# Kernel optimization log

Measured on AMD Instinct MI355X. Metric: run time of the kernel, lower is better.

## Reference

```python
import jax, jax.numpy as jnp
import numpy as np

S, N, F, H, O = 64, 4096, 32, 64, 2  # seq_len, n_nodes, nfeat, nhid, nout


def setup_inputs() -> dict:
    key = jax.random.key(0)
    ks = jax.random.split(key, 8)
    sc = 0.02
    return {
        "x": jax.random.normal(ks[0], (S, N, F), jnp.float32),
        "adj": jax.random.uniform(ks[1], (N, N), jnp.float32) / N,  # dense normalized-ish adjacency
        "W1": jax.random.normal(ks[2], (F, H), jnp.float32) * sc,
        "b1": jnp.zeros((H,), jnp.float32),
        "W2": jax.random.normal(ks[3], (H, O), jnp.float32) * sc,
        "b2": jnp.zeros((O,), jnp.float32),
        "Wih0": jax.random.normal(ks[4], (3 * H, O * N), jnp.float32) * sc,
        "Whh0": jax.random.normal(ks[5], (3 * H, H), jnp.float32) * sc,
        "bih0": jnp.zeros((3 * H,), jnp.float32),
        "bhh0": jnp.zeros((3 * H,), jnp.float32),
        "Wih1": jax.random.normal(ks[6], (3 * H, H), jnp.float32) * sc,
        "Whh1": jax.random.normal(ks[7], (3 * H, H), jnp.float32) * sc,
        "bih1": jnp.zeros((3 * H,), jnp.float32),
        "bhh1": jnp.zeros((3 * H,), jnp.float32),
    }


def _gru_layer(xs, Wih, Whh, bih, bhh):
    # xs: (S, B, in); PyTorch GRU cell semantics, h0 = 0
    B = xs.shape[1]
    h0 = jnp.zeros((B, Whh.shape[1]), xs.dtype)

    def step(h, x_t):
        gi = x_t @ Wih.T + bih            # (B, 3H)
        gh = h @ Whh.T + bhh              # (B, 3H)
        ir, iz, inn = jnp.split(gi, 3, axis=-1)
        hr, hz, hn = jnp.split(gh, 3, axis=-1)
        r = jax.nn.sigmoid(ir + hr)
        z = jax.nn.sigmoid(iz + hz)
        n = jnp.tanh(inn + r * hn)
        h_new = (1.0 - z) * n + z * h
        return h_new, h_new

    hT, ys = jax.lax.scan(step, h0, xs)
    return ys, hT


def reference(x, adj, W1, b1, W2, b2, Wih0, Whh0, bih0, bhh0, Wih1, Whh1, bih1, bhh1):
    # GCN per timestep (vectorized over time): adj @ (x @ W) + b, relu, adj @ (. @ W2) + b2, log_softmax
    # dropout inactive (eval mode)
    support = jnp.einsum('snf,fh->snh', x, W1) + b1          # (S, N, H)
    h = jnp.einsum('ij,sjh->sih', adj, support)              # (S, N, H)
    h = jax.nn.relu(h)
    support2 = jnp.einsum('snh,ho->sno', h, W2) + b2         # (S, N, O)
    g = jnp.einsum('ij,sjo->sio', adj, support2)             # (S, N, O)
    logp = jax.nn.log_softmax(g, axis=-1)                    # dim=1 of (N, O) per node
    rnn_in = logp.reshape(S, 1, N * O)                       # batch = 1 (torch.stack construction)
    ys0, h0T = _gru_layer(rnn_in, Wih0, Whh0, bih0, bhh0)
    ys1, h1T = _gru_layer(ys0, Wih1, Whh1, bih1, bhh1)
    hn = jnp.stack([h0T, h1T])                               # (n_layers, 1, H)
    return ys1, hn
```

## Files before the change

### kernel.cpp

```cpp
#include <hip/hip_runtime.h>
#include <stdint.h>

#define SS 64
#define NN 4096
#define FF 32
#define HH 64
#define OO 2
#define G3 192

typedef float f32x4 __attribute__((ext_vector_type(4)));
typedef short bf16x8 __attribute__((ext_vector_type(8)));
typedef unsigned short u16x8 __attribute__((ext_vector_type(8)));
typedef long longx2 __attribute__((ext_vector_type(2)));

#define AS1 __attribute__((address_space(1)))
#define AS3 __attribute__((address_space(3)))

__device__ __forceinline__ unsigned short f2bf(float f) {
  union { float f; uint32_t u; } v; v.f = f;
  uint32_t u = v.u;
  uint32_t r = (u + 0x7FFFu + ((u >> 16) & 1u)) >> 16;
  return (unsigned short)r;
}
__device__ __forceinline__ float bf2f(unsigned short s) {
  union { uint32_t u; float f; } v; v.u = ((uint32_t)s) << 16;
  return v.f;
}
__device__ __forceinline__ unsigned char f2e4m3(float x) {
  float a = fabsf(x);
  unsigned s = (x < 0.f) ? 0x80u : 0u;
  if (a >= 448.f) return (unsigned char)(s | 0x7E);
  if (a < 0.015625f) {
    int q = (int)rintf(a * 512.f);
    return (unsigned char)(s | (unsigned)q);
  }
  union { float f; uint32_t u; } v; v.f = a;
  uint32_t b = v.u + 0x7FFFFu + ((v.u >> 20) & 1u);
  int e = (int)(b >> 23) - 127;
  if (e > 8) return (unsigned char)(s | 0x7E);
  return (unsigned char)(s | (unsigned)(((e + 7) << 3) | ((b >> 20) & 7u)));
}
__device__ __forceinline__ int kperm_idx(int i) {
  int o8 = (i >> 3) & 7;
  int np = ((o8 & 3) << 1) | (o8 >> 2);
  return (i & ~63) | (np << 3) | (i & 7);
}

__global__ __launch_bounds__(256) void k_prep(const float* __restrict__ adj,
                                              unsigned char* __restrict__ adj8,
                                              float* __restrict__ rowsum,
                                              const float* __restrict__ x,
                                              unsigned char* __restrict__ Xt8) {
  __shared__ float xl[64][33];
  __shared__ float ps[4];
  int tid = threadIdx.x;
  if (blockIdx.x < 4096) {
    int row = blockIdx.x;
    const float4* src = (const float4*)(adj + (size_t)row * 4096);
    uchar4* dst8 = (uchar4*)(adj8 + (size_t)row * 4096);
    float sum = 0.f;
    #pragma unroll
    for (int q = 0; q < 4; ++q) {
      int idx = q * 256 + tid;
      float4 v = src[idx];
      uchar4 r8;
      r8.x = f2e4m3(v.x * 4096.f); r8.y = f2e4m3(v.y * 4096.f);
      r8.z = f2e4m3(v.z * 4096.f); r8.w = f2e4m3(v.w * 4096.f);
      int o8 = (idx >> 1) & 7;
      int np = ((o8 & 3) << 1) | (o8 >> 2);
      int nidx = (idx & ~15) | (np << 1) | (idx & 1);
      dst8[nidx] = r8;
      sum += (v.x + v.y) + (v.z + v.w);
    }
    #pragma unroll
    for (int off = 1; off < 64; off <<= 1) sum += __shfl_xor(sum, off);
    if ((tid & 63) == 0) ps[tid >> 6] = sum;
    __syncthreads();
    if (tid == 0) rowsum[row] = (ps[0] + ps[1]) + (ps[2] + ps[3]);
    return;
  }
  int bs = blockIdx.x - 4096;
  int s = bs >> 6, jb = (bs & 63) << 6;
  const float4* xg = (const float4*)(x + ((size_t)s * NN + jb) * FF);
  #pragma unroll
  for (int ii = 0; ii < 2; ++ii) {
    int idx = tid + ii * 256;
    float4 v = xg[idx];
    int j = idx >> 3, f = (idx & 7) << 2;
    xl[j][f] = v.x; xl[j][f + 1] = v.y; xl[j][f + 2] = v.z; xl[j][f + 3] = v.w;
  }
  __syncthreads();
  int f = tid >> 3, jc = tid & 7;
  unsigned int lo = 0, hi = 0;
  #pragma unroll
  for (int jj = 0; jj < 4; ++jj) lo |= ((unsigned int)f2e4m3(xl[jc * 8 + jj][f])) << (jj * 8);
  #pragma unroll
  for (int jj = 0; jj < 4; ++jj) hi |= ((unsigned int)f2e4m3(xl[jc * 8 + 4 + jj][f])) << (jj * 8);
  uint2 ov; ov.x = lo; ov.y = hi;
  int np = ((jc & 3) << 1) | (jc >> 2);
  *(uint2*)(Xt8 + (size_t)(s * 32 + f) * 4096 + jb + np * 8) = ov;
}

#define SBAR()   asm volatile("s_barrier" ::: "memory")
#define VMC9()   asm volatile("s_waitcnt vmcnt(9)" ::: "memory")
#define VMC6()   asm volatile("s_waitcnt vmcnt(6)" ::: "memory")
#define VMC4()   asm volatile("s_waitcnt vmcnt(4)" ::: "memory")
#define VMC3()   asm volatile("s_waitcnt vmcnt(3)" ::: "memory")
#define VMC0()   asm volatile("s_waitcnt vmcnt(0)" ::: "memory")

__global__ __launch_bounds__(512, 2) void k_gemmAX(
    const unsigned char* __restrict__ A8,
    const unsigned char* __restrict__ B8,
    const float* __restrict__ rowsum,
    const float* __restrict__ W1f,
    const float* __restrict__ b1f,
    const float* __restrict__ W2f,
    const float* __restrict__ b2f,
    unsigned char* __restrict__ B2t8) {
  __shared__ __align__(16) char lds[122880];
  __shared__ __align__(16) unsigned short w1t[64 * 40];
  __shared__ float w2l[128];
  __shared__ float b1l[64];
  __shared__ float b2l[2];
  const int tid = threadIdx.x;
  const int wid = tid >> 6, l = tid & 63;
  const int wr2 = wid >> 2, wc2 = wid & 3;
  const int lc = l & 15, lq = l >> 4;

  {
    float4 v = ((const float4*)W1f)[tid];
    int f = tid >> 4, h = (tid & 15) * 4;
    w1t[(h + 0) * 40 + f] = f2bf(v.x);
    w1t[(h + 1) * 40 + f] = f2bf(v.y);
    w1t[(h + 2) * 40 + f] = f2bf(v.z);
    w1t[(h + 3) * 40 + f] = f2bf(v.w);
  }
  if (tid < 32) *(float4*)&w2l[tid * 4] = ((const float4*)W2f)[tid];
  if (tid < 16) *(float4*)&b1l[tid * 4] = ((const float4*)b1f)[tid];
  if (tid < 2) b2l[tid] = b2f[tid];
  __syncthreads();

  int bid = blockIdx.x;
  int swz = (bid & 7) * 32 + (bid >> 3);
  const int i0 = (swz >> 3) * 128;
  const int c0 = (swz & 7) * 256;

  const int aBase = (wr2 * 64 + lc) * 64;
  const int bBase = 8192 + (wc2 * 64 + lc) * 64;
  const int aswz = (lc & 3) ^ ((lc >> 2) & 3);
  const int ckx = ((lq ^ aswz) << 4);

  const int srow = wid * 16 + (l >> 2);
  const int sswz = (srow & 3) ^ ((srow >> 2) & 3);
  const int scol = (((l & 3) ^ sswz) << 4);
  const char* gA = (const char*)A8 + (size_t)(i0 + srow) * 4096 + scol;
  const char* gB = (const char*)B8 + (size_t)(c0 + srow) * 4096 + scol;
  char* ldsW = (char*)lds + wid * 1024;
  const char* ldsR = (const char*)lds;

  f32x4 acc[4][4];
  #pragma unroll
  for (int m = 0; m < 4; ++m)
    #pragma unroll
    for (int n = 0; n < 4; ++n) acc[m][n] = {0.f, 0.f, 0.f, 0.f};

  longx2 afq[4], bfq[4];

#define STAGE3(KT, BOFS) do {                                                        \
    __builtin_amdgcn_global_load_lds((const AS1 void*)(gA + (KT) * 64),              \
        (AS3 void*)(ldsW + (BOFS)), 16, 0, 0);                                       \
    __builtin_amdgcn_global_load_lds((const AS1 void*)(gB + (KT) * 64),              \
        (AS3 void*)(ldsW + (BOFS) + 8192), 16, 0, 0);                                \
    __builtin_amdgcn_global_load_lds((const AS1 void*)(gB + 524288 + (KT) * 64),     \
        (AS3 void*)(ldsW + (BOFS) + 16384), 16, 0, 0);                               \
  } while (0)

#define READ_FR(BOFS) do {                                                           \
    _Pragma("unroll")                                                                \
    for (int _m = 0; _m < 4; ++_m)                                                   \
      afq[_m] = *(const longx2*)(ldsR + (BOFS) + aBase + _m * 1024 + ckx);           \
    _Pragma("unroll")                                                                \
    for (int _n = 0; _n < 4; ++_n)                                                   \
      bfq[_n] = *(const longx2*)(ldsR + (BOFS) + bBase + _n * 1024 + ckx);           \
  } while (0)

#define MFMA32() do {                                                                \
    __builtin_amdgcn_s_setprio(1);                                                   \
    _Pragma("unroll")                                                                \
    for (int _kk = 0; _kk < 2; ++_kk)                                                \
      _Pragma("unroll")                                                              \
      for (int _m = 0; _m < 4; ++_m)                                                 \
        _Pragma("unroll")                                                            \
        for (int _n = 0; _n < 4; ++_n)                                               \
          acc[_m][_n] = __builtin_amdgcn_mfma_f32_16x16x32_fp8_fp8(                  \
              afq[_m][_kk], bfq[_n][_kk], acc[_m][_n], 0, 0, 0);                     \
    __builtin_amdgcn_s_setprio(0);                                                   \
  } while (0)

  STAGE3(0, 0);
  STAGE3(1, 24576);
  STAGE3(2, 49152);
  STAGE3(3, 73728);
  VMC9();
  SBAR();

  int bR = 0, bS = 98304;
  for (int kt = 0; kt < 60; ++kt) {
    READ_FR(bR);
    STAGE3(kt + 4, bS);
    MFMA32();
    VMC9();
    SBAR();
    bR = (bR == 98304) ? 0 : bR + 24576;
    bS = (bS == 98304) ? 0 : bS + 24576;
  }
  READ_FR(bR); MFMA32(); VMC6(); SBAR(); bR = (bR == 98304) ? 0 : bR + 24576;
  READ_FR(bR); MFMA32(); VMC3(); SBAR(); bR = (bR == 98304) ? 0 : bR + 24576;
  READ_FR(bR); MFMA32(); VMC0(); SBAR(); bR = (bR == 98304) ? 0 : bR + 24576;
  READ_FR(bR); MFMA32();
  __syncthreads();

  unsigned short* C1L = (unsigned short*)lds;
  {
    const int rb = wr2 * 64 + lq * 4;
    const int cbL = wc2 * 64 + lc;
    #pragma unroll
    for (int m = 0; m < 4; ++m)
      #pragma unroll
      for (int r = 0; r < 4; ++r) {
        const int row = rb + m * 16 + r;
        #pragma unroll
        for (int n = 0; n < 4; ++n)
          C1L[row * 264 + cbL + n * 16] = f2bf(acc[m][n][r] * 0.000244140625f);
      }
  }
  __syncthreads();

  {
    const f32x4 zacc = {0.f, 0.f, 0.f, 0.f};
    bf16x8 bw[4];
    float b1v[4], w2a[4], w2b[4];
    #pragma unroll
    for (int n = 0; n < 4; ++n) {
      const int h = n * 16 + lc;
      bw[n] = *(const bf16x8*)((const char*)w1t + h * 80 + lq * 16);
      b1v[n] = b1l[h];
      w2a[n] = w2l[h * 2];
      w2b[n] = w2l[h * 2 + 1];
    }
    const int rbase = wid * 16 + lq * 4;
    const float4 rs4 = *(const float4*)&rowsum[i0 + rbase];
    const float bo0 = b2l[0], bo1 = b2l[1];
    #pragma unroll
    for (int s = 0; s < 8; ++s) {
      bf16x8 afe = *(const bf16x8*)((const char*)C1L +
                     (wid * 16 + lc) * 528 + s * 64 + lq * 16);
      float o0r[4] = {0.f, 0.f, 0.f, 0.f};
      float o1r[4] = {0.f, 0.f, 0.f, 0.f};
      #pragma unroll
      for (int n = 0; n < 4; ++n) {
        f32x4 hq = __builtin_amdgcn_mfma_f32_16x16x32_bf16(afe, bw[n], zacc, 0, 0, 0);
        #pragma unroll
        for (int r = 0; r < 4; ++r) {
          float hv = hq[r] + rs4[r] * b1v[n];
          hv = hv > 0.f ? hv : 0.f;
          o0r[r] += hv * w2a[n];
          o1r[r] += hv * w2b[n];
        }
      }
      #pragma unroll
      for (int off = 1; off < 16; off <<= 1)
        #pragma unroll
        for (int r = 0; r < 4; ++r) {
          o0r[r] += __shfl_xor(o0r[r], off);
          o1r[r] += __shfl_xor(o1r[r], off);
        }
      if (lc == 0) {
        const int sg = (c0 >> 5) + s;
        #pragma unroll
        for (int r = 0; r < 4; ++r) {
          const int ip = kperm_idx(i0 + rbase + r);
          B2t8[(size_t)(sg * 2 + 0) * 4096 + ip] = f2e4m3((o0r[r] + bo0) * 4096.f);
          B2t8[(size_t)(sg * 2 + 1) * 4096 + ip] = f2e4m3((o1r[r] + bo1) * 4096.f);
        }
      }
    }
  }
}

__global__ __launch_bounds__(256) void k_gemm2f8(
    const unsigned char* __restrict__ A8,
    const unsigned char* __restrict__ B8,
    float* __restrict__ Gp) {
  __shared__ __align__(16) char lds[49152];
  const int tid = threadIdx.x;
  const int wid = tid >> 6, l = tid & 63;
  const int wr = wid >> 1, wc = wid & 1;
  const int lc = l & 15, lq = l >> 4;
  const int bi = blockIdx.x & 31, ks = blockIdx.x >> 5;
  const int i0 = bi * 128;
  const size_t kbase = (size_t)ks * 512;

  const int aBase = (wr * 64 + lc) * 64;
  const int bBase = 8192 + (wc * 64 + lc) * 64;
  const int aswz = (lc & 3) ^ ((lc >> 2) & 3);
  const int ckx = ((lq ^ aswz) << 4);

  const int srow = wid * 16 + (l >> 2);
  const int sswz = (srow & 3) ^ ((srow >> 2) & 3);
  const int scol = (((l & 3) ^ sswz) << 4);
  const char* gA = (const char*)A8 + (size_t)(i0 + srow) * 4096 + kbase + scol;
  const char* gB = (const char*)B8 + (size_t)srow * 4096 + kbase + scol;
  char* ldsW = (char*)lds + wid * 1024;
  const char* ldsR = (const char*)lds;

  f32x4 acc[4][4];
  #pragma unroll
  for (int m = 0; m < 4; ++m)
    #pragma unroll
    for (int n = 0; n < 4; ++n) acc[m][n] = {0.f, 0.f, 0.f, 0.f};

  longx2 afq[4], bfq[4];

#define G2STAGE(KT, BOFS) do {                                                       \
    __builtin_amdgcn_global_load_lds((const AS1 void*)(gA + (KT) * 64),              \
        (AS3 void*)(ldsW + (BOFS)), 16, 0, 0);                                       \
    __builtin_amdgcn_global_load_lds((const AS1 void*)(gA + 262144 + (KT) * 64),     \
        (AS3 void*)(ldsW + (BOFS) + 4096), 16, 0, 0);                                \
    __builtin_amdgcn_global_load_lds((const AS1 void*)(gB + (KT) * 64),              \
        (AS3 void*)(ldsW + (BOFS) + 8192), 16, 0, 0);                                \
    __builtin_amdgcn_global_load_lds((const AS1 void*)(gB + 262144 + (KT) * 64),     \
        (AS3 void*)(ldsW + (BOFS) + 12288), 16, 0, 0);                               \
  } while (0)

#define G2READ(BOFS) do {                                                            \
    _Pragma("unroll")                                                                \
    for (int _m = 0; _m < 4; ++_m)                                                   \
      afq[_m] = *(const longx2*)(ldsR + (BOFS) + aBase + _m * 1024 + ckx);           \
    _Pragma("unroll")                                                                \
    for (int _n = 0; _n < 4; ++_n)                                                   \
      bfq[_n] = *(const longx2*)(ldsR + (BOFS) + bBase + _n * 1024 + ckx);           \
  } while (0)

#define G2MFMA() do {                                                                \
    __builtin_amdgcn_s_setprio(1);                                                   \
    _Pragma("unroll")                                                                \
    for (int _kk = 0; _kk < 2; ++_kk)                                                \
      _Pragma("unroll")                                                              \
      for (int _m = 0; _m < 4; ++_m)                                                 \
        _Pragma("unroll")                                                            \
        for (int _n = 0; _n < 4; ++_n)                                               \
          acc[_m][_n] = __builtin_amdgcn_mfma_f32_16x16x32_fp8_fp8(                  \
              afq[_m][_kk], bfq[_n][_kk], acc[_m][_n], 0, 0, 0);                     \
    __builtin_amdgcn_s_setprio(0);                                                   \
  } while (0)

  G2STAGE(0, 0);
  G2STAGE(1, 16384);
  VMC4();
  SBAR();

  int bR = 0, bS = 32768;
  for (int kt = 0; kt < 6; ++kt) {
    G2READ(bR);
    G2STAGE(kt + 2, bS);
    G2MFMA();
    VMC4();
    SBAR();
    bR = (bR == 32768) ? 0 : bR + 16384;
    bS = (bS == 32768) ? 0 : bS + 16384;
  }
  G2READ(bR); G2MFMA(); VMC0(); SBAR(); bR = (bR == 32768) ? 0 : bR + 16384;
  G2READ(bR); G2MFMA();

  float* outp = Gp + (size_t)ks * 524288;
  const int rbase = i0 + wr * 64 + lq * 4;
  const int cbase = wc * 64 + lc;
  #pragma unroll
  for (int m = 0; m < 4; ++m)
    #pragma unroll
    for (int n = 0; n < 4; ++n)
      #pragma unroll
      for (int r = 0; r < 4; ++r)
        outp[(size_t)(rbase + m * 16 + r) * 128 + cbase + n * 16] =
            acc[m][n][r] * 5.9604644775390625e-8f;
}

__global__ __launch_bounds__(256) void k_lsm(const float* __restrict__ Gp,
                                             float* __restrict__ Rm) {
  __shared__ float Gacc[32][130];
  int i0 = blockIdx.x * 32;
  int tid = threadIdx.x;
  float4 v[4];
  #pragma unroll
  for (int i = 0; i < 4; ++i) v[i] = {0.f, 0.f, 0.f, 0.f};
  for (int ks = 0; ks < 8; ++ks) {
    const float4* gp4 = ((const float4*)Gp) + (size_t)ks * 131072 + (size_t)i0 * 32;
    #pragma unroll
    for (int i = 0; i < 4; ++i) {
      float4 t = gp4[tid + i * 256];
      v[i].x += t.x; v[i].y += t.y; v[i].z += t.z; v[i].w += t.w;
    }
  }
  #pragma unroll
  for (int i = 0; i < 4; ++i) {
    int f4i = tid + i * 256, row = f4i >> 5, c = (f4i & 31) * 4;
    Gacc[row][c] = v[i].x; Gacc[row][c + 1] = v[i].y;
    Gacc[row][c + 2] = v[i].z; Gacc[row][c + 3] = v[i].w;
  }
  __syncthreads();
  #pragma unroll
  for (int j = 0; j < 8; ++j) {
    int p = j * 256 + tid;
    int ii = p & 31, s = p >> 5;
    float g0 = Gacc[ii][s * 2], g1 = Gacc[ii][s * 2 + 1];
    float m = fmaxf(g0, g1);
    float lse = m + logf(expf(g0 - m) + expf(g1 - m));
    float2 o_; o_.x = g0 - lse; o_.y = g1 - lse;
    *((float2*)(Rm + (size_t)s * 8192 + (size_t)(i0 + ii) * 2)) = o_;
  }
}

__global__ __launch_bounds__(256) void k_gi0(const float* __restrict__ Rm,
                                             const float* __restrict__ Wih0,
                                             float* __restrict__ part) {
  __shared__ float4 Wl[4 * 128];
  int gb = blockIdx.x % 48, ks = blockIdx.x / 48;
  int c0 = ks * 512;
  int tid = threadIdx.x;
  #pragma unroll
  for (int i = 0; i < 2; ++i) {
    int idx = tid + i * 256;
    int g = idx >> 7, c4 = idx & 127;
    Wl[g * 128 + c4] = ((const float4*)(Wih0 + (size_t)(gb * 4 + g) * 8192 + c0))[c4];
  }
  __syncthreads();
  int w = tid >> 6, lane = tid & 63;
  for (int pass = 0; pass < 16; ++pass) {
    int t = pass * 4 + w;
    float a0 = 0.f, a1 = 0.f, a2 = 0.f, a3 = 0.f;
    const float4* rg = (const float4*)(Rm + (size_t)t * 8192 + c0);
    #pragma unroll
    for (int i = 0; i < 2; ++i) {
      int c4 = i * 64 + lane;
      float4 r4 = rg[c4];
      float4 w0 = Wl[c4], w1 = Wl[128 + c4], w2 = Wl[256 + c4], w3 = Wl[384 + c4];
      a0 += r4.x * w0.x + r4.y * w0.y + r4.z * w0.z + r4.w * w0.w;
      a1 += r4.x * w1.x + r4.y * w1.y + r4.z * w1.z + r4.w * w1.w;
      a2 += r4.x * w2.x + r4.y * w2.y + r4.z * w2.z + r4.w * w2.w;
      a3 += r4.x * w3.x + r4.y * w3.y + r4.z * w3.z + r4.w * w3.w;
    }
    #pragma unroll
    for (int off = 1; off < 64; off <<= 1) {
      a0 += __shfl_xor(a0, off);
      a1 += __shfl_xor(a1, off);
      a2 += __shfl_xor(a2, off);
      a3 += __shfl_xor(a3, off);
    }
    if (lane == 0) {
      float4 o_; o_.x = a0; o_.y = a1; o_.z = a2; o_.w = a3;
      *((float4*)(part + ((size_t)ks * 64 + t) * 192 + gb * 4)) = o_;
    }
  }
}

__global__ __launch_bounds__(256) void k_gi0red(const float* __restrict__ part,
                                                const float* __restrict__ bih0,
                                                float* __restrict__ gi0) {
  int idx = blockIdx.x * 256 + threadIdx.x;
  if (idx < 12288) {
    float s_ = bih0[idx % 192];
    for (int ks = 0; ks < 16; ++ks) s_ += part[ks * 12288 + idx];
    gi0[idx] = s_;
  }
}

__device__ __forceinline__ float fsigm(float x) {
  return __builtin_amdgcn_rcpf(1.f + __expf(-x));
}
__device__ __forceinline__ float ftanh(float x) {
  return 1.f - 2.f * __builtin_amdgcn_rcpf(1.f + __expf(2.f * x));
}

__global__ __launch_bounds__(384) void k_gru(const float* __restrict__ gi0,
                                             const float* __restrict__ Whh0,
                                             const float* __restrict__ bhh0,
                                             const float* __restrict__ Wih1,
                                             const float* __restrict__ Whh1,
                                             const float* __restrict__ bih1,
                                             const float* __restrict__ bhh1,
                                             float* __restrict__ out) {
  __shared__ float gil[64][192];
  __shared__ float gout[576];
  __shared__ __align__(16) unsigned short hv[2][64];
  const int tid = threadIdx.x;
  const int w = tid >> 6, l = tid & 63;
  const int matw = w >> 1, half = w & 1;
  const float* Wm = (matw == 0) ? Whh0 : (matw == 1 ? Wih1 : Whh1);
  const int mi = (matw == 2) ? 1 : 0;

  bf16x8 afr[6][2];
  #pragma unroll
  for (int rbi = 0; rbi < 6; ++rbi) {
    int g = (half * 6 + rbi) * 16 + (l & 15);
    #pragma unroll
    for (int kh = 0; kh < 2; ++kh) {
      int k0 = kh * 32 + (l >> 4) * 8;
      const float4* src = (const float4*)(Wm + (size_t)g * 64 + k0);
      float4 v0 = src[0], v1 = src[1];
      bf16x8 a;
      a[0] = (short)f2bf(v0.x); a[1] = (short)f2bf(v0.y);
      a[2] = (short)f2bf(v0.z); a[3] = (short)f2bf(v0.w);
      a[4] = (short)f2bf(v1.x); a[5] = (short)f2bf(v1.y);
      a[6] = (short)f2bf(v1.z); a[7] = (short)f2bf(v1.w);
      afr[rbi][kh] = a;
    }
  }
  {
    float4* gf = (float4*)&gil[0][0];
    const float4* gs = (const float4*)gi0;
    #pragma unroll
    for (int i = 0; i < 8; ++i) gf[i * 384 + tid] = gs[i * 384 + tid];
  }
  if (tid < 128) hv[tid >> 6][tid & 63] = 0;

  float hreg = 0.f;
  float bR = 0.f, bZ = 0.f, bNa = 0.f, bNb = 0.f;
  if (tid < 64) {
    bR = bhh0[tid]; bZ = bhh0[64 + tid]; bNa = bhh0[128 + tid];
  } else if (tid < 128) {
    int g = tid - 64;
    bR = bih1[g] + bhh1[g];
    bZ = bih1[64 + g] + bhh1[64 + g];
    bNa = bih1[128 + g];
    bNb = bhh1[128 + g];
  }
  asm volatile("s_waitcnt lgkmcnt(0)\n\ts_barrier" ::: "memory");

  const int gwb = matw * 192 + half * 96 + (l >> 4) * 4;
  const f32x4 zacc = {0.f, 0.f, 0.f, 0.f};

  for (int i = 0; i <= 64; ++i) {
    bf16x8 b0 = *(const bf16x8*)&hv[mi][(l >> 4) * 8];
    bf16x8 b1 = *(const bf16x8*)&hv[mi][32 + (l >> 4) * 8];
    #pragma unroll
    for (int rbi = 0; rbi < 6; ++rbi) {
      f32x4 a_ = __builtin_amdgcn_mfma_f32_16x16x32_bf16(afr[rbi][0], b0, zacc, 0, 0, 0);
      a_ = __builtin_amdgcn_mfma_f32_16x16x32_bf16(afr[rbi][1], b1, a_, 0, 0, 0);
      if (!(l & 15)) *(f32x4*)&gout[gwb + rbi * 16] = a_;
    }
    asm volatile("s_waitcnt lgkmcnt(0)\n\ts_barrier" ::: "memory");
    if (tid < 64) {
      if (i < 64) {
        float r = fsigm(gil[i][tid] + gout[tid] + bR);
        float z = fsigm(gil[i][64 + tid] + gout[64 + tid] + bZ);
        float n = ftanh(gil[i][128 + tid] + r * (gout[128 + tid] + bNa));
        hreg = (1.f - z) * n + z * hreg;
        hv[0][tid] = f2bf(hreg);
      }
    } else if (tid < 128 && i > 0) {
      int g = tid - 64;
      float r = fsigm(gout[192 + g] + gout[384 + g] + bR);
      float z = fsigm(gout[256 + g] + gout[448 + g] + bZ);
      float n = ftanh((gout[320 + g] + bNa) + r * (gout[512 + g] + bNb));
      hreg = (1.f - z) * n + z * hreg;
      hv[1][g] = f2bf(hreg);
      out[(i - 1) * 64 + g] = hreg;
    }
    asm volatile("s_waitcnt lgkmcnt(0)\n\ts_barrier" ::: "memory");
  }
  if (tid < 64) out[4096 + tid] = hreg;
  else if (tid < 128) out[4096 + 64 + (tid - 64)] = hreg;
}

extern "C" void kernel_launch(void* const* d_in, const int* in_sizes, int n_in,
                              void* d_out, int out_size, void* d_ws, size_t ws_size,
                              hipStream_t stream) {
  const float* x    = (const float*)d_in[0];
  const float* adj  = (const float*)d_in[1];
  const float* W1   = (const float*)d_in[2];
  const float* b1   = (const float*)d_in[3];
  const float* W2   = (const float*)d_in[4];
  const float* b2   = (const float*)d_in[5];
  const float* Wih0 = (const float*)d_in[6];
  const float* Whh0 = (const float*)d_in[7];
  const float* bih0 = (const float*)d_in[8];
  const float* bhh0 = (const float*)d_in[9];
  const float* Wih1 = (const float*)d_in[10];
  const float* Whh1 = (const float*)d_in[11];
  const float* bih1 = (const float*)d_in[12];
  const float* bhh1 = (const float*)d_in[13];
  float* out = (float*)d_out;

  char* ws = (char*)d_ws;
  unsigned char* adj8  = (unsigned char*)ws;
  unsigned char* Xt8   = (unsigned char*)(ws + 16777216);
  float* rowsum        = (float*)(ws + 25165824);
  float* Gp            = (float*)(ws + 25182208);
  float* Rm            = (float*)(ws + 41959424);
  float* part          = (float*)(ws + 44056576);
  float* gi0           = (float*)(ws + 44843008);
  unsigned char* B2t8  = (unsigned char*)(ws + 44892160);

  k_prep<<<8192, 256, 0, stream>>>(adj, adj8, rowsum, x, Xt8);
  k_gemmAX<<<256, 512, 0, stream>>>(adj8, Xt8, rowsum, W1, b1, W2, b2, B2t8);
  k_gemm2f8<<<256, 256, 0, stream>>>(adj8, B2t8, Gp);
  k_lsm<<<128, 256, 0, stream>>>(Gp, Rm);
  k_gi0<<<768, 256, 0, stream>>>(Rm, Wih0, part);
  k_gi0red<<<48, 256, 0, stream>>>(part, bih0, gi0);
  k_gru<<<1, 384, 0, stream>>>(gi0, Whh0, bhh0, Wih1, Whh1, bih1, bhh1, out);
}
```

Baseline: 151.5 us.

## Double the K-tile to 128 in both fp8 GEMMs with 3-stage LDS ring

Result: no change. 148.9 us (-1.7%).

```diff
diff --git a/kernel.cpp b/kernel.cpp
--- a/kernel.cpp
+++ b/kernel.cpp
@@ -40,10 +40,10 @@
   if (e > 8) return (unsigned char)(s | 0x7E);
   return (unsigned char)(s | (unsigned)(((e + 7) << 3) | ((b >> 20) & 7u)));
 }
-__device__ __forceinline__ int kperm_idx(int i) {
-  int o8 = (i >> 3) & 7;
-  int np = ((o8 & 3) << 1) | (o8 >> 2);
-  return (i & ~63) | (np << 3) | (i & 7);
+__device__ __forceinline__ int kperm128(int i) {
+  int b = (i >> 3) & 15;
+  int np = ((b & 7) << 1) | (b >> 3);
+  return (i & ~127) | (np << 3) | (i & 7);
 }
 
 __global__ __launch_bounds__(256) void k_prep(const float* __restrict__ adj,
@@ -66,9 +66,9 @@
       uchar4 r8;
       r8.x = f2e4m3(v.x * 4096.f); r8.y = f2e4m3(v.y * 4096.f);
       r8.z = f2e4m3(v.z * 4096.f); r8.w = f2e4m3(v.w * 4096.f);
-      int o8 = (idx >> 1) & 7;
-      int np = ((o8 & 3) << 1) | (o8 >> 2);
-      int nidx = (idx & ~15) | (np << 1) | (idx & 1);
+      int b = (idx >> 1) & 15;
+      int np = ((b & 7) << 1) | (b >> 3);
+      int nidx = (idx & ~31) | (np << 1) | (idx & 1);
       dst8[nidx] = r8;
       sum += (v.x + v.y) + (v.z + v.w);
     }
@@ -97,15 +97,13 @@
   #pragma unroll
   for (int jj = 0; jj < 4; ++jj) hi |= ((unsigned int)f2e4m3(xl[jc * 8 + 4 + jj][f])) << (jj * 8);
   uint2 ov; ov.x = lo; ov.y = hi;
-  int np = ((jc & 3) << 1) | (jc >> 2);
-  *(uint2*)(Xt8 + (size_t)(s * 32 + f) * 4096 + jb + np * 8) = ov;
+  int np = (jc << 1) | ((jb >> 6) & 1);
+  *(uint2*)(Xt8 + (size_t)(s * 32 + f) * 4096 + (jb & ~127) + np * 8) = ov;
 }
 
 #define SBAR()   asm volatile("s_barrier" ::: "memory")
-#define VMC9()   asm volatile("s_waitcnt vmcnt(9)" ::: "memory")
+#define VMC8()   asm volatile("s_waitcnt vmcnt(8)" ::: "memory")
 #define VMC6()   asm volatile("s_waitcnt vmcnt(6)" ::: "memory")
-#define VMC4()   asm volatile("s_waitcnt vmcnt(4)" ::: "memory")
-#define VMC3()   asm volatile("s_waitcnt vmcnt(3)" ::: "memory")
 #define VMC0()   asm volatile("s_waitcnt vmcnt(0)" ::: "memory")
 
 __global__ __launch_bounds__(512, 2) void k_gemmAX(
@@ -117,7 +115,7 @@
     const float* __restrict__ W2f,
     const float* __restrict__ b2f,
     unsigned char* __restrict__ B2t8) {
-  __shared__ __align__(16) char lds[122880];
+  __shared__ __align__(16) char lds[147456];
   __shared__ __align__(16) unsigned short w1t[64 * 40];
   __shared__ float w2l[128];
   __shared__ float b1l[64];
@@ -145,14 +143,13 @@
   const int i0 = (swz >> 3) * 128;
   const int c0 = (swz & 7) * 256;
 
-  const int aBase = (wr2 * 64 + lc) * 64;
-  const int bBase = 8192 + (wc2 * 64 + lc) * 64;
-  const int aswz = (lc & 3) ^ ((lc >> 2) & 3);
-  const int ckx = ((lq ^ aswz) << 4);
-
-  const int srow = wid * 16 + (l >> 2);
-  const int sswz = (srow & 3) ^ ((srow >> 2) & 3);
-  const int scol = (((l & 3) ^ sswz) << 4);
+  const int aBase = (wr2 * 64 + lc) * 128;
+  const int bBase = 16384 + (wc2 * 64 + lc) * 128;
+  const int cLo = ((lq ^ (lc & 7)) << 4);
+  const int cHi = (((4 + lq) ^ (lc & 7)) << 4);
+
+  const int srow = wid * 8 + (l >> 3);
+  const int scol = (((l & 7) ^ (srow & 7)) << 4);
   const char* gA = (const char*)A8 + (size_t)(i0 + srow) * 4096 + scol;
   const char* gB = (const char*)B8 + (size_t)(c0 + srow) * 4096 + scol;
   char* ldsW = (char*)lds + wid * 1024;
@@ -166,25 +163,31 @@
 
   longx2 afq[4], bfq[4];
 
-#define STAGE3(KT, BOFS) do {                                                        \
-    __builtin_amdgcn_global_load_lds((const AS1 void*)(gA + (KT) * 64),              \
+#define STAGE6(KT, BOFS) do {                                                        \
+    __builtin_amdgcn_global_load_lds((const AS1 void*)(gA + (KT) * 128),             \
         (AS3 void*)(ldsW + (BOFS)), 16, 0, 0);                                       \
-    __builtin_amdgcn_global_load_lds((const AS1 void*)(gB + (KT) * 64),              \
+    __builtin_amdgcn_global_load_lds((const AS1 void*)(gA + 262144 + (KT) * 128),    \
         (AS3 void*)(ldsW + (BOFS) + 8192), 16, 0, 0);                                \
-    __builtin_amdgcn_global_load_lds((const AS1 void*)(gB + 524288 + (KT) * 64),     \
+    __builtin_amdgcn_global_load_lds((const AS1 void*)(gB + (KT) * 128),             \
         (AS3 void*)(ldsW + (BOFS) + 16384), 16, 0, 0);                               \
+    __builtin_amdgcn_global_load_lds((const AS1 void*)(gB + 262144 + (KT) * 128),    \
+        (AS3 void*)(ldsW + (BOFS) + 24576), 16, 0, 0);                               \
+    __builtin_amdgcn_global_load_lds((const AS1 void*)(gB + 524288 + (KT) * 128),    \
+        (AS3 void*)(ldsW + (BOFS) + 32768), 16, 0, 0);                               \
+    __builtin_amdgcn_global_load_lds((const AS1 void*)(gB + 786432 + (KT) * 128),    \
+        (AS3 void*)(ldsW + (BOFS) + 40960), 16, 0, 0);                               \
   } while (0)
 
-#define READ_FR(BOFS) do {                                                           \
+#define READ_CH(BOFS, CK) do {                                                       \
     _Pragma("unroll")                                                                \
     for (int _m = 0; _m < 4; ++_m)                                                   \
-      afq[_m] = *(const longx2*)(ldsR + (BOFS) + aBase + _m * 1024 + ckx);           \
+      afq[_m] = *(const longx2*)(ldsR + (BOFS) + aBase + _m * 2048 + (CK));          \
     _Pragma("unroll")                                                                \
     for (int _n = 0; _n < 4; ++_n)                                                   \
-      bfq[_n] = *(const longx2*)(ldsR + (BOFS) + bBase + _n * 1024 + ckx);           \
+      bfq[_n] = *(const longx2*)(ldsR + (BOFS) + bBase + _n * 2048 + (CK));          \
   } while (0)
 
-#define MFMA32() do {                                                                \
+#define MFMA2K() do {                                                                \
     __builtin_amdgcn_s_setprio(1);                                                   \
     _Pragma("unroll")                                                                \
     for (int _kk = 0; _kk < 2; ++_kk)                                                \
@@ -197,27 +200,26 @@
     __builtin_amdgcn_s_setprio(0);                                                   \
   } while (0)
 
-  STAGE3(0, 0);
-  STAGE3(1, 24576);
-  STAGE3(2, 49152);
-  STAGE3(3, 73728);
-  VMC9();
+  STAGE6(0, 0);
+  STAGE6(1, 49152);
+  VMC6();
   SBAR();
 
   int bR = 0, bS = 98304;
-  for (int kt = 0; kt < 60; ++kt) {
-    READ_FR(bR);
-    STAGE3(kt + 4, bS);
-    MFMA32();
-    VMC9();
+  for (int kt = 0; kt < 30; ++kt) {
+    READ_CH(bR, cLo);
+    STAGE6(kt + 2, bS);
+    MFMA2K();
+    READ_CH(bR, cHi);
+    MFMA2K();
+    VMC6();
     SBAR();
-    bR = (bR == 98304) ? 0 : bR + 24576;
-    bS = (bS == 98304) ? 0 : bS + 24576;
-  }
-  READ_FR(bR); MFMA32(); VMC6(); SBAR(); bR = (bR == 98304) ? 0 : bR + 24576;
-  READ_FR(bR); MFMA32(); VMC3(); SBAR(); bR = (bR == 98304) ? 0 : bR + 24576;
-  READ_FR(bR); MFMA32(); VMC0(); SBAR(); bR = (bR == 98304) ? 0 : bR + 24576;
-  READ_FR(bR); MFMA32();
+    bR = (bR == 98304) ? 0 : bR + 49152;
+    bS = (bS == 98304) ? 0 : bS + 49152;
+  }
+  READ_CH(bR, cLo); MFMA2K(); READ_CH(bR, cHi); MFMA2K();
+  VMC0(); SBAR(); bR = (bR == 98304) ? 0 : bR + 49152;
+  READ_CH(bR, cLo); MFMA2K(); READ_CH(bR, cHi); MFMA2K();
   __syncthreads();
 
   unsigned short* C1L = (unsigned short*)lds;
@@ -279,7 +281,7 @@
         const int sg = (c0 >> 5) + s;
         #pragma unroll
         for (int r = 0; r < 4; ++r) {
-          const int ip = kperm_idx(i0 + rbase + r);
+          const int ip = kperm128(i0 + rbase + r);
           B2t8[(size_t)(sg * 2 + 0) * 4096 + ip] = f2e4m3((o0r[r] + bo0) * 4096.f);
           B2t8[(size_t)(sg * 2 + 1) * 4096 + ip] = f2e4m3((o1r[r] + bo1) * 4096.f);
         }
@@ -292,7 +294,7 @@
     const unsigned char* __restrict__ A8,
     const unsigned char* __restrict__ B8,
     float* __restrict__ Gp) {
-  __shared__ __align__(16) char lds[49152];
+  __shared__ __align__(16) char lds[98304];
   const int tid = threadIdx.x;
   const int wid = tid >> 6, l = tid & 63;
   const int wr = wid >> 1, wc = wid & 1;
@@ -301,14 +303,13 @@
   const int i0 = bi * 128;
   const size_t kbase = (size_t)ks * 512;
 
-  const int aBase = (wr * 64 + lc) * 64;
-  const int bBase = 8192 + (wc * 64 + lc) * 64;
-  const int aswz = (lc & 3) ^ ((lc >> 2) & 3);
-  const int ckx = ((lq ^ aswz) << 4);
-
-  const int srow = wid * 16 + (l >> 2);
-  const int sswz = (srow & 3) ^ ((srow >> 2) & 3);
-  const int scol = (((l & 3) ^ sswz) << 4);
+  const int aBase = (wr * 64 + lc) * 128;
+  const int bBase = 16384 + (wc * 64 + lc) * 128;
+  const int cLo = ((lq ^ (lc & 7)) << 4);
+  const int cHi = (((4 + lq) ^ (lc & 7)) << 4);
+
+  const int srow = wid * 8 + (l >> 3);
+  const int scol = (((l & 7) ^ (srow & 7)) << 4);
   const char* gA = (const char*)A8 + (size_t)(i0 + srow) * 4096 + kbase + scol;
   const char* gB = (const char*)B8 + (size_t)srow * 4096 + kbase + scol;
   char* ldsW = (char*)lds + wid * 1024;
@@ -323,23 +324,31 @@
   longx2 afq[4], bfq[4];
 
 #define G2STAGE(KT, BOFS) do {                                                       \
-    __builtin_amdgcn_global_load_lds((const AS1 void*)(gA + (KT) * 64),              \
+    __builtin_amdgcn_global_load_lds((const AS1 void*)(gA + (KT) * 128),             \
         (AS3 void*)(ldsW + (BOFS)), 16, 0, 0);                                       \
-    __builtin_amdgcn_global_load_lds((const AS1 void*)(gA + 262144 + (KT) * 64),     \
+    __builtin_amdgcn_global_load_lds((const AS1 void*)(gA + 131072 + (KT) * 128),    \
         (AS3 void*)(ldsW + (BOFS) + 4096), 16, 0, 0);                                \
-    __builtin_amdgcn_global_load_lds((const AS1 void*)(gB + (KT) * 64),              \
+    __builtin_amdgcn_global_load_lds((const AS1 void*)(gA + 262144 + (KT) * 128),    \
         (AS3 void*)(ldsW + (BOFS) + 8192), 16, 0, 0);                                \
-    __builtin_amdgcn_global_load_lds((const AS1 void*)(gB + 262144 + (KT) * 64),     \
+    __builtin_amdgcn_global_load_lds((const AS1 void*)(gA + 393216 + (KT) * 128),    \
         (AS3 void*)(ldsW + (BOFS) + 12288), 16, 0, 0);                               \
+    __builtin_amdgcn_global_load_lds((const AS1 void*)(gB + (KT) * 128),             \
+        (AS3 void*)(ldsW + (BOFS) + 16384), 16, 0, 0);                               \
+    __builtin_amdgcn_global_load_lds((const AS1 void*)(gB + 131072 + (KT) * 128),    \
+        (AS3 void*)(ldsW + (BOFS) + 20480), 16, 0, 0);                               \
+    __builtin_amdgcn_global_load_lds((const AS1 void*)(gB + 262144 + (KT) * 128),    \
+        (AS3 void*)(ldsW + (BOFS) + 24576), 16, 0, 0);                               \
+    __builtin_amdgcn_global_load_lds((const AS1 void*)(gB + 393216 + (KT) * 128),    \
+        (AS3 void*)(ldsW + (BOFS) + 28672), 16, 0, 0);                               \
   } while (0)
 
-#define G2READ(BOFS) do {                                                            \
+#define G2READ(BOFS, CK) do {                                                        \
     _Pragma("unroll")                                                                \
     for (int _m = 0; _m < 4; ++_m)                                                   \
-      afq[_m] = *(const longx2*)(ldsR + (BOFS) + aBase + _m * 1024 + ckx);           \
+      afq[_m] = *(const longx2*)(ldsR + (BOFS) + aBase + _m * 2048 + (CK));          \
     _Pragma("unroll")                                                                \
     for (int _n = 0; _n < 4; ++_n)                                                   \
-      bfq[_n] = *(const longx2*)(ldsR + (BOFS) + bBase + _n * 1024 + ckx);           \
+      bfq[_n] = *(const longx2*)(ldsR + (BOFS) + bBase + _n * 2048 + (CK));          \
   } while (0)
 
 #define G2MFMA() do {                                                                \
@@ -356,22 +365,17 @@
   } while (0)
 
   G2STAGE(0, 0);
-  G2STAGE(1, 16384);
-  VMC4();
+  G2STAGE(1, 32768);
+  VMC8();
   SBAR();
 
-  int bR = 0, bS = 32768;
-  for (int kt = 0; kt < 6; ++kt) {
-    G2READ(bR);
-    G2STAGE(kt + 2, bS);
-    G2MFMA();
-    VMC4();
-    SBAR();
-    bR = (bR == 32768) ? 0 : bR + 16384;
-    bS = (bS == 32768) ? 0 : bS + 16384;
-  }
-  G2READ(bR); G2MFMA(); VMC0(); SBAR(); bR = (bR == 32768) ? 0 : bR + 16384;
-  G2READ(bR); G2MFMA();
+  G2READ(0, cLo); G2STAGE(2, 65536); G2MFMA(); G2READ(0, cHi); G2MFMA();
+  VMC8(); SBAR();
+  G2READ(32768, cLo); G2STAGE(3, 0); G2MFMA(); G2READ(32768, cHi); G2MFMA();
+  VMC8(); SBAR();
+  G2READ(65536, cLo); G2MFMA(); G2READ(65536, cHi); G2MFMA();
+  VMC0(); SBAR();
+  G2READ(0, cLo); G2MFMA(); G2READ(0, cHi); G2MFMA();
 
   float* outp = Gp + (size_t)ks * 524288;
   const int rbase = i0 + wr * 64 + lq * 4;
```
